# Optimization experiments

Hardware: AMD Instinct MI355X
Metric: run time of the kernel (lower is better)

## Reference

```python
import jax, jax.numpy as jnp
import numpy as np

NEG_INF = -1000000000.0


def setup_inputs() -> dict:
    key = jax.random.key(0)
    k1, k2, k3, k4, k5 = jax.random.split(key, 5)
    B, L1, L2, F1, F2, A = 64, 1024, 1024, 128, 128, 128
    feature1 = jax.random.normal(k1, (B, L1, F1), dtype=jnp.float32)
    feature2 = jax.random.normal(k2, (B, L2, F2), dtype=jnp.float32)
    mask = jax.random.randint(k3, (B, L1, L2), 0, 2, dtype=jnp.int32)
    # Linear weights stored torch-style: [out_features, in_features]
    W1 = jax.random.normal(k4, (A, F1), dtype=jnp.float32) / np.sqrt(F1)
    b1 = jnp.zeros((A,), dtype=jnp.float32)
    W2 = jax.random.normal(k5, (A, F2), dtype=jnp.float32) / np.sqrt(F2)
    b2 = jnp.zeros((A,), dtype=jnp.float32)
    return {"feature1": feature1, "feature2": feature2, "mask": mask,
            "W1": W1, "b1": b1, "W2": W2, "b2": b2}


def reference(feature1, feature2, mask, W1, b1, W2, b2):
    A = W1.shape[0]
    scale = jnp.sqrt(jnp.float32(A))
    q = jnp.einsum('bld,ad->bla', feature1, W1) + b1  # [B, L1, A]
    k = jnp.einsum('bmd,ad->bma', feature2, W2) + b2  # [B, L2, A]
    a = jnp.einsum('bla,bma->blm', q, k) / scale       # [B, L1, L2]
    masked_a = jnp.where(mask == 0, NEG_INF, a)
    alpha1 = jax.nn.softmax(masked_a, axis=2)  # softmax over L2
    alpha2 = jax.nn.softmax(masked_a, axis=1)  # softmax over L1
    out1 = jnp.einsum('blm,blf->bmf', alpha2, feature1)  # [B, L2, F1]
    out2 = jnp.einsum('blm,bmf->blf', alpha1, feature2)  # [B, L1, F2]
    return (out1, out2)
```

## Files before the change

### kernel.cpp

```cpp
#include <hip/hip_runtime.h>
#include <stdint.h>

typedef _Float16 f16;
typedef f16 f16x4 __attribute__((ext_vector_type(4)));
typedef f16 f16x8 __attribute__((ext_vector_type(8)));
typedef float f32x4 __attribute__((ext_vector_type(4)));

constexpr float SCALE = 0.08838834764831845f;

__device__ __forceinline__ void glds16(const void* g, void* l) {
  __builtin_amdgcn_global_load_lds(
      (const __attribute__((address_space(1))) void*)g,
      (__attribute__((address_space(3))) void*)l, 16, 0, 0);
}
__device__ __forceinline__ void glds4(const void* g, void* l) {
  __builtin_amdgcn_global_load_lds(
      (const __attribute__((address_space(1))) void*)g,
      (__attribute__((address_space(3))) void*)l, 4, 0, 0);
}

__global__ __launch_bounds__(256) void pack_kernel(
    const int* __restrict__ mask, uint32_t* __restrict__ bits)
{
  const int wv = blockIdx.x * 4 + (threadIdx.x >> 6);
  const int lane = threadIdx.x & 63;
  const size_t e0 = (size_t)wv * 8192;
  const int4* src = (const int4*)(mask + e0) + lane;
  uint32_t* wout = bits + (e0 >> 5);
#pragma unroll 4
  for (int it = 0; it < 32; ++it) {
    int4 v = src[it * 64];
    uint32_t nib = (v.x ? 1u : 0u) | (v.y ? 2u : 0u) | (v.z ? 4u : 0u) | (v.w ? 8u : 0u);
    uint32_t p = nib | (__shfl_xor((int)nib, 1) << 4);
    p = p | ((uint32_t)__shfl_xor((int)p, 2) << 8);
    p = p | ((uint32_t)__shfl_xor((int)p, 4) << 16);
    if ((lane & 7) == 0) wout[it * 8 + (lane >> 3)] = p;
  }
}

__global__ __launch_bounds__(256) void proj_kernel(
    const float* __restrict__ f1, const float* __restrict__ f2,
    const float* __restrict__ W1, const float* __restrict__ b1,
    const float* __restrict__ W2, const float* __restrict__ b2,
    f16* __restrict__ q_h, f16* __restrict__ k_h,
    f16* __restrict__ f1t, f16* __restrict__ f2t)
{
  __shared__ f16 a_lds[128 * 128];
  __shared__ f16 w_lds[128 * 128];

  const int tid = threadIdx.x;
  const int blk = blockIdx.x;
  const bool qside = blk < 512;
  const float* feat = qside ? f1 : f2;
  const float* W    = qside ? W1 : W2;
  const float* bias = qside ? b1 : b2;
  f16* op = qside ? q_h : k_h;
  f16* ft = qside ? f1t : f2t;
  const size_t row0 = (size_t)(qside ? blk : blk - 512) * 128;

  for (int it = 0; it < 16; ++it) {
    int u = tid + it * 256;
    int r = u >> 5;
    int c4 = (u & 31) * 4;
    float4 v = *(const float4*)&feat[(row0 + r) * 128 + c4];
    f16x4 h4 = { (f16)v.x, (f16)v.y, (f16)v.z, (f16)v.w };
    int adr = r * 128 + ((((c4 >> 3) ^ (r & 7)) << 3) | (c4 & 7));
    *(f16x4*)&a_lds[adr] = h4;
    float4 wv = *(const float4*)&W[r * 128 + c4];
    f16x4 wh = { (f16)wv.x, (f16)wv.y, (f16)wv.z, (f16)wv.w };
    *(f16x4*)&w_lds[adr] = wh;
  }
  __syncthreads();

  const int w = tid >> 6, l = tid & 63, lam = l & 15, g = l >> 4;
  f32x4 acc[2][8] = {};
#pragma unroll
  for (int kc = 0; kc < 4; ++kc) {
    f16x8 a[2];
#pragma unroll
    for (int rf = 0; rf < 2; ++rf) {
      int ar = w * 32 + rf * 16 + lam;
      a[rf] = *(const f16x8*)&a_lds[ar * 128 + (((4 * kc + g) ^ (ar & 7)) << 3)];
    }
#pragma unroll
    for (int cf = 0; cf < 8; ++cf) {
      int br = cf * 16 + lam;
      f16x8 bfr = *(const f16x8*)&w_lds[br * 128 + (((4 * kc + g) ^ (br & 7)) << 3)];
      acc[0][cf] = __builtin_amdgcn_mfma_f32_16x16x32_f16(a[0], bfr, acc[0][cf], 0, 0, 0);
      acc[1][cf] = __builtin_amdgcn_mfma_f32_16x16x32_f16(a[1], bfr, acc[1][cf], 0, 0, 0);
    }
  }
#pragma unroll
  for (int cf = 0; cf < 8; ++cf) {
    int col = cf * 16 + lam;
    float bv = bias[col];
#pragma unroll
    for (int rf = 0; rf < 2; ++rf)
#pragma unroll
      for (int i = 0; i < 4; ++i) {
        size_t grow = row0 + w * 32 + rf * 16 + g * 4 + i;
        op[grow * 128 + col] = (f16)(acc[rf][cf][i] + bv);
      }
  }

  {
    const int b = (int)(row0 >> 10);
    const int l0 = (int)(row0 & 1023);
    const int f = tid >> 1;
    const int half = tid & 1;
    f16 buf[64];
#pragma unroll
    for (int j = 0; j < 64; ++j) {
      int r = half * 64 + j;
      buf[j] = a_lds[r * 128 + ((((f >> 3) ^ (r & 7)) << 3) | (f & 7))];
    }
    f16* dst = ft + ((size_t)b * 128 + f) * 1024 + l0 + half * 64;
#pragma unroll
    for (int c = 0; c < 8; ++c)
      *(f16x8*)&dst[c * 8] = *(const f16x8*)&buf[c * 8];
  }
}

template <int PASS>
__global__ __launch_bounds__(256, 2) void attn_kernel(
    const f16* __restrict__ Qh, const f16* __restrict__ Kh,
    const f16* __restrict__ Vt, const uint32_t* __restrict__ bits,
    float* __restrict__ outp)
{
  __shared__ f16 k_lds[64 * 128];
  __shared__ f16 v_lds[128 * 64];
  __shared__ f16 p_lds[8 * 16 * 72];
  __shared__ uint32_t mb[256];

  const int tid = threadIdx.x;
  const int u = blockIdx.x;
  const int qt = (u >> 3) & 7;
  const int b = ((u >> 6) << 3) | (u & 7);
  const int w = tid >> 6, l = tid & 63, lam = l & 15, g = l >> 4;
  const size_t batch_row = (size_t)b << 10;

  f16x8 qf[2][4];
#pragma unroll
  for (int qd = 0; qd < 2; ++qd) {
    const f16* qbase = Qh + (batch_row + qt * 128 + w * 32 + qd * 16 + lam) * 128;
#pragma unroll
    for (int kc = 0; kc < 4; ++kc) qf[qd][kc] = *(const f16x8*)&qbase[kc * 32 + g * 8];
  }

  f32x4 acc[2][8] = {};
  float mrun[2][4], lrun[2][4];
#pragma unroll
  for (int qd = 0; qd < 2; ++qd)
#pragma unroll
    for (int i = 0; i < 4; ++i) { mrun[qd][i] = -__builtin_inff(); lrun[qd][i] = 0.f; }

  const f16* vtb = Vt + ((size_t)b << 17);

  for (int kt = 0; kt < 16; ++kt) {
    const int kb = kt * 64;
    __syncthreads();
    {
      const f16* kbase = Kh + (batch_row + kb) * 128;
#pragma unroll
      for (int it = 0; it < 4; ++it) {
        int slot0 = (w * 4 + it) * 64;
        int i = slot0 + l;
        int r = i >> 4, ch = i & 15;
        glds16(kbase + r * 128 + ((ch ^ (r & 7)) << 3), &k_lds[slot0 * 8]);
      }
    }
    {
#pragma unroll
      for (int it = 0; it < 4; ++it) {
        int slot0 = (w * 4 + it) * 64;
        int i = slot0 + l;
        int r = i >> 3, ch = i & 7;
        glds16(vtb + r * 1024 + kb + ((ch ^ (r & 7)) << 3), &v_lds[slot0 * 8]);
      }
    }
    {
      int idx = w * 64 + l;
      const uint32_t* src;
      if constexpr (PASS == 0)
        src = bits + (batch_row + qt * 128 + (idx >> 1)) * 32 + kt * 2 + (l & 1);
      else
        src = bits + (batch_row + kb + (idx >> 2)) * 32 + qt * 4 + (l & 3);
      glds4(src, &mb[w * 64]);
    }
    __syncthreads();

#pragma unroll
    for (int qd = 0; qd < 2; ++qd) {
      f32x4 sv[4] = {};
      __builtin_amdgcn_s_setprio(1);
#pragma unroll
      for (int kc = 0; kc < 4; ++kc) {
#pragma unroll
        for (int cf = 0; cf < 4; ++cf) {
          int br = cf * 16 + lam;
          f16x8 bk = *(const f16x8*)&k_lds[br * 128 + (((4 * kc + g) ^ (br & 7)) << 3)];
          sv[cf] = __builtin_amdgcn_mfma_f32_16x16x32_f16(qf[qd][kc], bk, sv[cf], 0, 0, 0);
        }
      }
      __builtin_amdgcn_s_setprio(0);

      uint32_t mk = 0;
      if constexpr (PASS == 0) {
#pragma unroll
        for (int i = 0; i < 4; ++i) {
          int rowi = w * 32 + qd * 16 + g * 4 + i;
          uint32_t w0 = mb[rowi * 2 + 0];
          uint32_t w1 = mb[rowi * 2 + 1];
#pragma unroll
          for (int cf = 0; cf < 4; ++cf) {
            uint32_t wd = (cf < 2) ? w0 : w1;
            mk |= ((wd >> ((cf & 1) * 16 + lam)) & 1u) << (cf * 4 + i);
          }
        }
      } else {
#pragma unroll
        for (int cf = 0; cf < 4; ++cf) {
          uint32_t wd = mb[(cf * 16 + lam) * 4 + w];
#pragma unroll
          for (int i = 0; i < 4; ++i)
            mk |= ((wd >> (qd * 16 + g * 4 + i)) & 1u) << (cf * 4 + i);
        }
      }

      float mrow4[4];
#pragma unroll
      for (int i = 0; i < 4; ++i) mrow4[i] = -1e30f;
#pragma unroll
      for (int cf = 0; cf < 4; ++cf)
#pragma unroll
        for (int i = 0; i < 4; ++i) {
          float v = sv[cf][i] * SCALE;
          sv[cf][i] = v;
          mrow4[i] = fmaxf(mrow4[i], ((mk >> (cf * 4 + i)) & 1u) ? v : -1e30f);
        }
#pragma unroll
      for (int d = 1; d <= 8; d <<= 1)
#pragma unroll
        for (int i = 0; i < 4; ++i)
          mrow4[i] = fmaxf(mrow4[i], __shfl_xor(mrow4[i], d, 64));

      float sf[4], lsum[4];
#pragma unroll
      for (int i = 0; i < 4; ++i) {
        float mn = fmaxf(mrun[qd][i], mrow4[i]);
        sf[i] = __expf(mrun[qd][i] - mn);
        mrun[qd][i] = mn;
        lsum[i] = 0.f;
      }
      f16* pslice = &p_lds[(w * 2 + qd) * 1152];
#pragma unroll
      for (int cf = 0; cf < 4; ++cf)
#pragma unroll
        for (int i = 0; i < 4; ++i) {
          float p = ((mk >> (cf * 4 + i)) & 1u) ? __expf(sv[cf][i] - mrun[qd][i]) : 0.f;
          lsum[i] += p;
          int row = g * 4 + i;
          int cchunk = 2 * cf + (lam >> 3);
          pslice[row * 72 + (((cchunk ^ (row & 7)) << 3) | (lam & 7))] = (f16)p;
        }
#pragma unroll
      for (int d = 1; d <= 8; d <<= 1)
#pragma unroll
        for (int i = 0; i < 4; ++i)
          lsum[i] += __shfl_xor(lsum[i], d, 64);
#pragma unroll
      for (int i = 0; i < 4; ++i) lrun[qd][i] = lrun[qd][i] * sf[i] + lsum[i];
#pragma unroll
      for (int nf = 0; nf < 8; ++nf)
#pragma unroll
        for (int i = 0; i < 4; ++i) acc[qd][nf][i] *= sf[i];
    }

    __builtin_amdgcn_s_setprio(1);
#pragma unroll
    for (int kc2 = 0; kc2 < 2; ++kc2) {
      f16x8 ap0 = *(const f16x8*)&p_lds[(w * 2 + 0) * 1152 + lam * 72 + (((4 * kc2 + g) ^ (lam & 7)) << 3)];
      f16x8 ap1 = *(const f16x8*)&p_lds[(w * 2 + 1) * 1152 + lam * 72 + (((4 * kc2 + g) ^ (lam & 7)) << 3)];
#pragma unroll
      for (int nf = 0; nf < 8; ++nf) {
        int vr = nf * 16 + lam;
        f16x8 bv = *(const f16x8*)&v_lds[vr * 64 + (((kc2 * 4 + g) ^ (vr & 7)) << 3)];
        acc[0][nf] = __builtin_amdgcn_mfma_f32_16x16x32_f16(ap0, bv, acc[0][nf], 0, 0, 0);
        acc[1][nf] = __builtin_amdgcn_mfma_f32_16x16x32_f16(ap1, bv, acc[1][nf], 0, 0, 0);
      }
    }
    __builtin_amdgcn_s_setprio(0);
  }

#pragma unroll
  for (int qd = 0; qd < 2; ++qd) {
    float inv[4];
#pragma unroll
    for (int i = 0; i < 4; ++i) inv[i] = (lrun[qd][i] > 0.f) ? 1.f / lrun[qd][i] : 0.f;
    const size_t orow0 = batch_row + (size_t)qt * 128 + w * 32 + qd * 16;
#pragma unroll
    for (int nf = 0; nf < 8; ++nf)
#pragma unroll
      for (int i = 0; i < 4; ++i)
        outp[(orow0 + g * 4 + i) * 128 + nf * 16 + lam] = acc[qd][nf][i] * inv[i];
  }
}

extern "C" void kernel_launch(void* const* d_in, const int* in_sizes, int n_in,
                              void* d_out, int out_size, void* d_ws, size_t ws_size,
                              hipStream_t stream) {
  const float* f1 = (const float*)d_in[0];
  const float* f2 = (const float*)d_in[1];
  const int* mask = (const int*)d_in[2];
  const float* W1 = (const float*)d_in[3];
  const float* b1 = (const float*)d_in[4];
  const float* W2 = (const float*)d_in[5];
  const float* b2 = (const float*)d_in[6];
  float* out = (float*)d_out;

  if (ws_size < (size_t)3 * 8388608 * sizeof(f16) + 8388608) return;

  f16* q_h = (f16*)d_ws;
  f16* k_h = q_h + 8388608;
  f16* f1t = k_h + 8388608;
  uint32_t* bits = (uint32_t*)(f1t + 8388608);
  f16* f2t = (f16*)d_out;

  pack_kernel<<<2048, 256, 0, stream>>>(mask, bits);
  proj_kernel<<<1024, 256, 0, stream>>>(f1, f2, W1, b1, W2, b2, q_h, k_h, f1t, f2t);
  attn_kernel<0><<<512, 256, 0, stream>>>(q_h, k_h, f2t, bits, out + 8388608);
  attn_kernel<1><<<512, 256, 0, stream>>>(k_h, q_h, f1t, bits, out);
}
```

Measured before the change: 265.7 us.

## Repack mask bits into strided word layout with swizzled LDS mask tiles

The mask packing kernel now gives each lane one 32-bit word that gathers the nibbles of 8 consecutive int4 loads, with no cross-lane shuffles. The packed words therefore hold a strided, interleaved layout. The attention kernels load a larger XOR-swizzled LDS mask tile (4 KB instead of 1 KB) and decode bits with new indexing. In pass 1, 4 bits can now be extracted with a single shift and mask. This removes shuffle overhead in packing and simplifies the per-row bit extraction, at the cost of more LDS traffic and space, and the bit layout is fragile.

```diff
diff --git a/kernel.cpp b/kernel.cpp
--- a/kernel.cpp
+++ b/kernel.cpp
@@ -24,17 +24,19 @@
 {
   const int wv = blockIdx.x * 4 + (threadIdx.x >> 6);
   const int lane = threadIdx.x & 63;
-  const size_t e0 = (size_t)wv * 8192;
-  const int4* src = (const int4*)(mask + e0) + lane;
-  uint32_t* wout = bits + (e0 >> 5);
-#pragma unroll 4
-  for (int it = 0; it < 32; ++it) {
-    int4 v = src[it * 64];
-    uint32_t nib = (v.x ? 1u : 0u) | (v.y ? 2u : 0u) | (v.z ? 4u : 0u) | (v.w ? 8u : 0u);
-    uint32_t p = nib | (__shfl_xor((int)nib, 1) << 4);
-    p = p | ((uint32_t)__shfl_xor((int)p, 2) << 8);
-    p = p | ((uint32_t)__shfl_xor((int)p, 4) << 16);
-    if ((lane & 7) == 0) wout[it * 8 + (lane >> 3)] = p;
+#pragma unroll 2
+  for (int cc = 0; cc < 4; ++cc) {
+    const size_t c = (size_t)wv * 4 + cc;
+    const int4* src = (const int4*)(mask + c * 2048) + lane;
+    uint32_t word = 0;
+#pragma unroll
+    for (int it = 0; it < 8; ++it) {
+      int4 v = src[it * 64];
+      uint32_t nib = (v.x ? 1u : 0u) | (v.y ? 2u : 0u) |
+                     (v.z ? 4u : 0u) | (v.w ? 8u : 0u);
+      word |= nib << (it * 4);
+    }
+    bits[c * 64 + lane] = word;
   }
 }
 
@@ -130,7 +132,7 @@
   __shared__ f16 k_lds[64 * 128];
   __shared__ f16 v_lds[128 * 64];
   __shared__ f16 p_lds[8 * 16 * 72];
-  __shared__ uint32_t mb[256];
+  __shared__ uint32_t mb2[1024];
 
   const int tid = threadIdx.x;
   const int u = blockIdx.x;
@@ -179,13 +181,23 @@
       }
     }
     {
-      int idx = w * 64 + l;
-      const uint32_t* src;
-      if constexpr (PASS == 0)
-        src = bits + (batch_row + qt * 128 + (idx >> 1)) * 32 + kt * 2 + (l & 1);
-      else
-        src = bits + (batch_row + kb + (idx >> 2)) * 32 + qt * 4 + (l & 3);
-      glds4(src, &mb[w * 64]);
+      if constexpr (PASS == 0) {
+        const uint32_t* bw = bits + ((batch_row + qt * 128) >> 1) * 64 + (kt & 3) * 16;
+#pragma unroll
+        for (int t = 0; t < 4; ++t) {
+          int p = (w * 4 + t) * 64 + l;
+          glds4(bw + (p >> 4) * 64 + ((p & 15) ^ (((p >> 4) & 3) << 2)),
+                &mb2[(w * 4 + t) * 64]);
+        }
+      } else {
+        const uint32_t* bw = bits + ((batch_row + kb) >> 1) * 64 + (qt & 1) * 32;
+#pragma unroll
+        for (int t = 0; t < 4; ++t) {
+          int p = (w * 4 + t) * 64 + l;
+          glds4(bw + (p >> 5) * 64 + ((p & 31) ^ (((p >> 5) & 7) << 2)),
+                &mb2[(w * 4 + t) * 64]);
+        }
+      }
     }
     __syncthreads();
 
@@ -206,24 +218,25 @@
 
       uint32_t mk = 0;
       if constexpr (PASS == 0) {
-#pragma unroll
-        for (int i = 0; i < 4; ++i) {
-          int rowi = w * 32 + qd * 16 + g * 4 + i;
-          uint32_t w0 = mb[rowi * 2 + 0];
-          uint32_t w1 = mb[rowi * 2 + 1];
-#pragma unroll
-          for (int cf = 0; cf < 4; ++cf) {
-            uint32_t wd = (cf < 2) ? w0 : w1;
-            mk |= ((wd >> ((cf & 1) * 16 + lam)) & 1u) << (cf * 4 + i);
+        const int so = ((kt >> 2) << 2) + (lam & 3);
+#pragma unroll
+        for (int cf = 0; cf < 4; ++cf)
+#pragma unroll
+          for (int ih = 0; ih < 2; ++ih) {
+            int rp = w * 16 + qd * 8 + g * 2 + ih;
+            int s  = cf * 4 + (lam >> 2);
+            uint32_t wd = mb2[rp * 16 + (s ^ ((rp & 3) << 2))];
+            mk |= ((wd >> so) & 1u) << (cf * 4 + ih * 2);
+            mk |= ((wd >> (16 + so)) & 1u) << (cf * 4 + ih * 2 + 1);
           }
-        }
       } else {
+        const int shift = ((lam & 1) << 4) + ((qt >> 1) << 2);
+        const int s1 = w * 8 + qd * 4 + g;
 #pragma unroll
         for (int cf = 0; cf < 4; ++cf) {
-          uint32_t wd = mb[(cf * 16 + lam) * 4 + w];
-#pragma unroll
-          for (int i = 0; i < 4; ++i)
-            mk |= ((wd >> (qd * 16 + g * 4 + i)) & 1u) << (cf * 4 + i);
+          int rp = cf * 8 + (lam >> 1);
+          uint32_t wd = mb2[rp * 32 + (s1 ^ ((rp & 7) << 2))];
+          mk |= ((wd >> shift) & 15u) << (cf * 4);
         }
       }
 
```

Result: faster. 257.1 us (-3.2%).
